# Kernel tuning notes

Hardware: AMD Instinct MI355X
Metric: run time of the kernel (lower is better)

Reference implementation:

```python
import jax, jax.numpy as jnp
import numpy as np

B, C, N = 4, 16, 128
H_SET = 128   # set_layers[0]
D_OUT = 128   # channel_layers[0]


def setup_inputs() -> dict:
    key = jax.random.key(0)
    ks = jax.random.split(key, 7)
    x = jax.random.normal(ks[0], (B, C, N, N), dtype=jnp.float32)
    # phi: Linear(4 -> 128), ReLU, Linear(128 -> 2)
    W1 = jax.random.normal(ks[1], (H_SET, 4), dtype=jnp.float32) * 0.5
    b1 = jax.random.normal(ks[2], (H_SET,), dtype=jnp.float32) * 0.05
    W2 = jax.random.normal(ks[3], (2, H_SET), dtype=jnp.float32) * 0.1
    b2 = jax.random.normal(ks[4], (2,), dtype=jnp.float32) * 0.05
    # channel_fc: Conv2d(C -> 128, kernel 1) + ReLU  (1x1 conv == channel matmul)
    Wc = jax.random.normal(ks[5], (D_OUT, C), dtype=jnp.float32) * (1.0 / np.sqrt(C))
    bc = jax.random.normal(ks[6], (D_OUT,), dtype=jnp.float32) * 0.05
    return {"x": x, "W1": W1, "b1": b1, "W2": W2, "b2": b2, "Wc": Wc, "bc": bc}


def reference(x, W1, b1, W2, b2, Wc, bc):
    Bx, Cx, n, _ = x.shape
    ii = jnp.arange(n - 1)
    jj = jnp.arange(n)
    # group element g = i*n + j selects index pair (p, q) = (j, (j+i+1) mod n)
    p = jnp.broadcast_to(jj[None, :], (n - 1, n)).reshape(-1)        # (G,)
    q = ((jj[None, :] + ii[:, None] + 1) % n).reshape(-1)            # (G,)
    idx = jnp.stack([p, q], axis=-1)                                 # (G, 2)
    # gather 2x2 blocks: block[b,c,g] = x[b,c][[p,q]][:, [p,q]]
    block = x[:, :, idx[:, :, None], idx[:, None, :]]                # (B,C,G,2,2)
    v = block.reshape(Bx, Cx, -1, 4)                                 # (B,C,G,4)
    # phi: tiny per-element MLP 4 -> H -> 2
    h = jax.nn.relu(v @ W1.T + b1) @ W2.T + b2                       # (B,C,G,2)
    # scatter: off-diagonal entries get h[..., 1] at (p, q) (indices unique)
    out = jnp.zeros((Bx, Cx, n, n), x.dtype).at[:, :, p, q].set(h[..., 1])
    # diagonal: diag[j] = sum_i h[:, :, i*n + j, 0]
    diag = h[..., 0].reshape(Bx, Cx, n - 1, n).sum(axis=2)           # (B,C,n)
    ar = jnp.arange(n)
    out = out.at[:, :, ar, ar].add(diag)
    # coeff: 1 off-diagonal, 1/(n-1) on diagonal
    eye = jnp.eye(n, dtype=x.dtype)
    coeff = (1.0 - eye) + eye * (1.0 / (n - 1))
    out = out * coeff
    # channel_fc: 1x1 conv + ReLU
    y = jax.nn.relu(jnp.einsum('bcnm,dc->bdnm', out, Wc) + bc[None, :, None, None])
    return y
```

## Files before the change

### kernel.cpp

```cpp
#include <hip/hip_runtime.h>

#define NN 128
#define CCH 16
#define BB 4
#define HID 128
#define DOUT 128

typedef float v2f __attribute__((ext_vector_type(2)));

__global__ __launch_bounds__(1024, 8) void fused_rey(
    const float* __restrict__ x,
    const float* __restrict__ W1, const float* __restrict__ b1,
    const float* __restrict__ W2, const float* __restrict__ b2,
    const float* __restrict__ Wc, const float* __restrict__ bc,
    float* __restrict__ y)
{
    __shared__ float s_out[CCH][NN];
    __shared__ float s_diag[CCH];

    const int t    = threadIdx.x;
    const int bid0 = blockIdx.x;
    const int bid  = ((bid0 & 7) << 6) | (bid0 >> 3);
    const int p    = bid & 127;
    const int b    = bid >> 7;
    const int c    = t >> 6;
    const int lane = t & 63;
    const int q0   = lane * 2;

    const size_t mbase = (size_t)(b * CCH + c) << 14;
    const float* xm = x + mbase;

    const v2f xpq = *reinterpret_cast<const v2f*>(&xm[p * NN + q0]);
    const v2f xqp = { xm[q0 * NN + p], xm[(q0 + 1) * NN + p] };
    const v2f xqq = { xm[q0 * (NN + 1)], xm[(q0 + 1) * (NN + 1)] };
    const float xpp = xm[p * (NN + 1)];
    const v2f xpp2 = { xpp, xpp };

    const float bb0 = b2[0], bb1 = b2[1];
    const v2f z2 = { 0.f, 0.f };
    v2f h0 = z2, h1 = z2;

    #pragma unroll 4
    for (int k = 0; k < HID; ++k) {
        const float4 w  = reinterpret_cast<const float4*>(W1)[k];
        const float b1k = b1[k];
        const float w20 = W2[k];
        const float w21 = W2[HID + k];
        v2f hd = __builtin_elementwise_fma((v2f){ w.x, w.x }, xpp2, (v2f){ b1k, b1k });
        hd = __builtin_elementwise_fma((v2f){ w.y, w.y }, xpq, hd);
        hd = __builtin_elementwise_fma((v2f){ w.z, w.z }, xqp, hd);
        hd = __builtin_elementwise_fma((v2f){ w.w, w.w }, xqq, hd);
        hd = __builtin_elementwise_max(hd, z2);
        h0 = __builtin_elementwise_fma((v2f){ w20, w20 }, hd, h0);
        h1 = __builtin_elementwise_fma((v2f){ w21, w21 }, hd, h1);
    }

    const v2f o = h1 + (v2f){ bb1, bb1 };
    *reinterpret_cast<v2f*>(&s_out[c][q0]) = o;

    float s = ((q0 == p) ? 0.f : h0[0]) + ((q0 + 1 == p) ? 0.f : h0[1]);
    #pragma unroll
    for (int off = 32; off > 0; off >>= 1)
        s += __shfl_down(s, off, 64);
    if (lane == 0) s_diag[c] = s * (1.0f / (NN - 1)) + bb0;

    __syncthreads();
    if (t < CCH) s_out[t][p] = s_diag[t];
    __syncthreads();

    const int wv = t >> 6;
    const int m0 = lane * 2;
    v2f r[CCH];
    #pragma unroll
    for (int cc = 0; cc < CCH; ++cc)
        r[cc] = *reinterpret_cast<const v2f*>(&s_out[cc][m0]);

    #pragma unroll 2
    for (int dd = 0; dd < 8; ++dd) {
        const int d = wv * 8 + dd;
        const float bcv = bc[d];
        v2f acc = { bcv, bcv };
        #pragma unroll
        for (int cc = 0; cc < CCH; ++cc) {
            const float wcf = Wc[d * CCH + cc];
            acc = __builtin_elementwise_fma((v2f){ wcf, wcf }, r[cc], acc);
        }
        acc = __builtin_elementwise_max(acc, z2);
        *reinterpret_cast<v2f*>(
            &y[(((size_t)(b * DOUT + d)) * NN + p) * NN + m0]) = acc;
    }
}

extern "C" void kernel_launch(void* const* d_in, const int* in_sizes, int n_in,
                              void* d_out, int out_size, void* d_ws, size_t ws_size,
                              hipStream_t stream) {
    const float* x  = (const float*)d_in[0];
    const float* W1 = (const float*)d_in[1];
    const float* b1 = (const float*)d_in[2];
    const float* W2 = (const float*)d_in[3];
    const float* b2 = (const float*)d_in[4];
    const float* Wc = (const float*)d_in[5];
    const float* bc = (const float*)d_in[6];
    float* y = (float*)d_out;

    fused_rey<<<dim3(BB * NN), 1024, 0, stream>>>(x, W1, b1, W2, b2, Wc, bc, y);
}
```

Baseline: 36.58 us.

## Compute phi hidden layer with bf16 MFMA and halve block size

Moves the per-element 4->128 hidden-layer matmul onto bf16 MFMA instructions. The x_pp term plus bias is precomputed per channel into a shared table and fed in as the accumulator, and the W2 reductions are done in registers with cross-lane shuffles. Blocks shrink to 512 threads, each wave handling two channels and sixteen output channels in the 1x1 conv. This removes most of the scalar FMA work of the hidden layer, at the cost of bf16 rounding of x and W1 (with a 0.25 prescale) and the wasted zero-padded K slots in each MFMA.

```diff
diff --git a/kernel.cpp b/kernel.cpp
--- a/kernel.cpp
+++ b/kernel.cpp
@@ -6,9 +6,17 @@
 #define HID 128
 #define DOUT 128
 
-typedef float v2f __attribute__((ext_vector_type(2)));
+typedef float f32x4 __attribute__((ext_vector_type(4)));
+typedef short s16x8 __attribute__((ext_vector_type(8)));
+typedef float v2f   __attribute__((ext_vector_type(2)));
 
-__global__ __launch_bounds__(1024, 8) void fused_rey(
+__device__ __forceinline__ short bfr(float f) {
+    unsigned int u = __float_as_uint(f);
+    u += 0x7fffu + ((u >> 16) & 1u);
+    return (short)(u >> 16);
+}
+
+__global__ __launch_bounds__(512, 2) void fused_rey(
     const float* __restrict__ x,
     const float* __restrict__ W1, const float* __restrict__ b1,
     const float* __restrict__ W2, const float* __restrict__ b2,
@@ -16,6 +24,9 @@
     float* __restrict__ y)
 {
     __shared__ float s_out[CCH][NN];
+    __shared__ float a_tab[CCH][HID];
+    __shared__ float w20t[HID];
+    __shared__ float w21t[HID];
     __shared__ float s_diag[CCH];
 
     const int t    = threadIdx.x;
@@ -23,61 +34,104 @@
     const int bid  = ((bid0 & 7) << 6) | (bid0 >> 3);
     const int p    = bid & 127;
     const int b    = bid >> 7;
-    const int c    = t >> 6;
-    const int lane = t & 63;
-    const int q0   = lane * 2;
+    const int w    = t >> 6;
+    const int l    = t & 63;
+    const int lc   = l & 15;
+    const float bb0 = b2[0], bb1 = b2[1];
 
-    const size_t mbase = (size_t)(b * CCH + c) << 14;
-    const float* xm = x + mbase;
-
-    const v2f xpq = *reinterpret_cast<const v2f*>(&xm[p * NN + q0]);
-    const v2f xqp = { xm[q0 * NN + p], xm[(q0 + 1) * NN + p] };
-    const v2f xqq = { xm[q0 * (NN + 1)], xm[(q0 + 1) * (NN + 1)] };
-    const float xpp = xm[p * (NN + 1)];
-    const v2f xpp2 = { xpp, xpp };
-
-    const float bb0 = b2[0], bb1 = b2[1];
-    const v2f z2 = { 0.f, 0.f };
-    v2f h0 = z2, h1 = z2;
-
-    #pragma unroll 4
-    for (int k = 0; k < HID; ++k) {
-        const float4 w  = reinterpret_cast<const float4*>(W1)[k];
-        const float b1k = b1[k];
-        const float w20 = W2[k];
-        const float w21 = W2[HID + k];
-        v2f hd = __builtin_elementwise_fma((v2f){ w.x, w.x }, xpp2, (v2f){ b1k, b1k });
-        hd = __builtin_elementwise_fma((v2f){ w.y, w.y }, xpq, hd);
-        hd = __builtin_elementwise_fma((v2f){ w.z, w.z }, xqp, hd);
-        hd = __builtin_elementwise_fma((v2f){ w.w, w.w }, xqq, hd);
-        hd = __builtin_elementwise_max(hd, z2);
-        h0 = __builtin_elementwise_fma((v2f){ w20, w20 }, hd, h0);
-        h1 = __builtin_elementwise_fma((v2f){ w21, w21 }, hd, h1);
+    if (t < HID) { w20t[t] = W2[t]; w21t[t] = W2[HID + t]; }
+    #pragma unroll
+    for (int i = 0; i < 4; ++i) {
+        const int idx = t + 512 * i;
+        const int cc = idx >> 7, k = idx & 127;
+        const float xpp = x[(((size_t)(b * CCH + cc)) << 14) + p * (NN + 1)];
+        a_tab[cc][k] = fmaf(W1[4 * k], xpp, b1[k]);
     }
 
-    const v2f o = h1 + (v2f){ bb1, bb1 };
-    *reinterpret_cast<v2f*>(&s_out[c][q0]) = o;
+    s16x8 afrag[8];
+    #pragma unroll
+    for (int kt = 0; kt < 8; ++kt) {
+        const int k = kt * 16 + lc;
+        afrag[kt] = (s16x8){ bfr(0.25f * W1[4 * k + 1]),
+                             bfr(0.25f * W1[4 * k + 2]),
+                             bfr(0.25f * W1[4 * k + 3]), 0, 0, 0, 0, 0 };
+    }
 
-    float s = ((q0 == p) ? 0.f : h0[0]) + ((q0 + 1 == p) ? 0.f : h0[1]);
+    __syncthreads();
+
     #pragma unroll
-    for (int off = 32; off > 0; off >>= 1)
-        s += __shfl_down(s, off, 64);
-    if (lane == 0) s_diag[c] = s * (1.0f / (NN - 1)) + bb0;
+    for (int c2 = 0; c2 < 2; ++c2) {
+        const int c = w + 8 * c2;
+        const float* xm = x + (((size_t)(b * CCH + c)) << 14);
+
+        s16x8 bfrag[8];
+        #pragma unroll
+        for (int qt = 0; qt < 8; ++qt) {
+            const int q = qt * 16 + lc;
+            bfrag[qt] = (s16x8){ bfr(xm[p * NN + q]),
+                                 bfr(xm[q * NN + p]),
+                                 bfr(xm[q * (NN + 1)]), 0, 0, 0, 0, 0 };
+        }
+
+        float h0p[8], h1p[8];
+        #pragma unroll
+        for (int qt = 0; qt < 8; ++qt) { h0p[qt] = 0.f; h1p[qt] = 0.f; }
+
+        #pragma unroll
+        for (int kt = 0; kt < 8; ++kt) {
+            const int kb = kt * 16 + 4 * (l >> 4);
+            const float4 av  = *reinterpret_cast<const float4*>(&a_tab[c][kb]);
+            const float4 s20 = *reinterpret_cast<const float4*>(&w20t[kb]);
+            const float4 s21 = *reinterpret_cast<const float4*>(&w21t[kb]);
+            f32x4 ci; ci[0] = av.x; ci[1] = av.y; ci[2] = av.z; ci[3] = av.w;
+
+            #pragma unroll
+            for (int qt = 0; qt < 8; ++qt) {
+                f32x4 acc = __builtin_amdgcn_mfma_f32_16x16x32_bf16(
+                                afrag[kt], bfrag[qt], ci, 0, 0, 0);
+                const float u0 = fmaxf(acc[0], 0.f);
+                const float u1 = fmaxf(acc[1], 0.f);
+                const float u2 = fmaxf(acc[2], 0.f);
+                const float u3 = fmaxf(acc[3], 0.f);
+                float h0 = h0p[qt], h1 = h1p[qt];
+                h0 = fmaf(s20.x, u0, h0); h1 = fmaf(s21.x, u0, h1);
+                h0 = fmaf(s20.y, u1, h0); h1 = fmaf(s21.y, u1, h1);
+                h0 = fmaf(s20.z, u2, h0); h1 = fmaf(s21.z, u2, h1);
+                h0 = fmaf(s20.w, u3, h0); h1 = fmaf(s21.w, u3, h1);
+                h0p[qt] = h0; h1p[qt] = h1;
+            }
+        }
+
+        float dsum = 0.f;
+        #pragma unroll
+        for (int qt = 0; qt < 8; ++qt) {
+            float hq0 = h0p[qt], hq1 = h1p[qt];
+            hq0 += __shfl_xor(hq0, 16); hq0 += __shfl_xor(hq0, 32);
+            hq1 += __shfl_xor(hq1, 16); hq1 += __shfl_xor(hq1, 32);
+            const int q = qt * 16 + lc;
+            if (l < 16) s_out[c][q] = hq1 + bb1;
+            dsum += (q == p) ? 0.f : hq0;
+        }
+        #pragma unroll
+        for (int m = 8; m > 0; m >>= 1) dsum += __shfl_xor(dsum, m);
+        if (l == 0) s_diag[c] = dsum * (1.0f / (NN - 1)) + bb0;
+    }
 
     __syncthreads();
     if (t < CCH) s_out[t][p] = s_diag[t];
     __syncthreads();
 
     const int wv = t >> 6;
-    const int m0 = lane * 2;
+    const int m0 = l * 2;
+    const v2f z2 = { 0.f, 0.f };
     v2f r[CCH];
     #pragma unroll
     for (int cc = 0; cc < CCH; ++cc)
         r[cc] = *reinterpret_cast<const v2f*>(&s_out[cc][m0]);
 
-    #pragma unroll 2
-    for (int dd = 0; dd < 8; ++dd) {
-        const int d = wv * 8 + dd;
+    #pragma unroll 4
+    for (int dd = 0; dd < 16; ++dd) {
+        const int d = wv * 16 + dd;
         const float bcv = bc[d];
         v2f acc = { bcv, bcv };
         #pragma unroll
@@ -103,5 +157,5 @@
     const float* bc = (const float*)d_in[6];
     float* y = (float*)d_out;
 
-    fused_rey<<<dim3(BB * NN), 1024, 0, stream>>>(x, W1, b1, W2, b2, Wc, bc, y);
+    fused_rey<<<dim3(BB * NN), 512, 0, stream>>>(x, W1, b1, W2, b2, Wc, bc, y);
 }
```

Result: slower. 95.16 us (+160.2%).
